# Optimization experiments

Measured on AMD Instinct MI355X. Metric: run time of the kernel, lower is better.

The kernel has to match this reference:

```python
import jax, jax.numpy as jnp
import numpy as np

B, DIM, H, W = 128, 640, 10, 10
M = H * W


def setup_inputs() -> dict:
    key = jax.random.key(0)
    x = jax.random.normal(key, (B, DIM, M), dtype=jnp.float32)
    # learned temperature parameter, init = log(1 / (2*h*w)), shape (1, 1)
    t = jnp.log(1.0 / (2 * H * W) * jnp.ones((1, 1), dtype=jnp.float32))
    return {"x": x, "t": t}


def reference(x, t):
    # x: [B, dim, M], t: [1, 1] temperature (log-scale)
    dim = x.shape[1]
    # Gram matrix x x^T: [B, dim, dim]
    xxT = jnp.einsum('bdm,bem->bde', x, x)
    # I_M.bmm(x_pow2*I) and (x_pow2*I).bmm(I_M) are just diagonal broadcasts
    d = jnp.diagonal(xxT, axis1=1, axis2=2)  # [B, dim]
    dcov = d[:, None, :] + d[:, :, None] - 2.0 * xxT
    dcov = jnp.maximum(dcov, 1e-4)
    dcov = jnp.sqrt(jnp.exp(t) * dcov + 1e-5)
    # double centering: dcov.bmm(I_M)/dim == row means, I_M.bmm(dcov)/dim == col means
    row_mean = jnp.mean(dcov, axis=2, keepdims=True)   # [B, dim, 1]
    col_mean = jnp.mean(dcov, axis=1, keepdims=True)   # [B, 1, dim]
    tot_mean = jnp.mean(dcov, axis=(1, 2), keepdims=True)  # [B, 1, 1]
    out = dcov - row_mean - col_mean + tot_mean
    return out.reshape(out.shape[0], dim * dim)
```

## Files before the change

kernel.cpp:

```cpp
#include <hip/hip_runtime.h>
#include <cmath>

#define NB    128
#define DIM_  640
#define MM    100
#define XHR   128
#define LDK   136
#define TFS   68
#define TTS   66
#define RSS   34
#define CSS   10

#define NWG   (NB * 55)
#define CPX   (NWG / 8)

typedef _Float16 half8 __attribute__((ext_vector_type(8)));
typedef float f32x4 __attribute__((ext_vector_type(4)));

__device__ inline void decode_bp(int bid, int& b, int& p) {
    const int dec = (bid & 7) * CPX + (bid >> 3);
    b = dec / 55;
    p = dec - b * 55;
}

__global__ __launch_bounds__(256) void prep_xh(const float* __restrict__ x,
                                               _Float16* __restrict__ xh,
                                               float* __restrict__ d,
                                               float* __restrict__ rmz) {
    if (blockIdx.x < 321) {
        const int z = blockIdx.x * 256 + threadIdx.x;
        if (z < 82048) rmz[z] = 0.f;
    }
    const int row  = blockIdx.x * 4 + (threadIdx.x >> 6);
    const int lane = threadIdx.x & 63;
    const float* xr = x + (size_t)row * MM;
    float2 v = make_float2(0.f, 0.f);
    if (lane < 50) v = *(const float2*)(xr + 2 * lane);
    const _Float16 h0 = (_Float16)v.x, h1 = (_Float16)v.y;
    const float a0 = (float)h0, a1 = (float)h1;
    float acc = a0 * a0 + a1 * a1;
    union { _Float16 h[2]; unsigned u; } pk;
    pk.h[0] = h0; pk.h[1] = h1;
    *(unsigned*)(xh + (size_t)row * XHR + 2 * lane) = pk.u;
    #pragma unroll
    for (int off = 32; off; off >>= 1) acc += __shfl_down(acc, off, 64);
    if (lane == 0) d[row] = acc;
}

__device__ inline void stage_xh(const _Float16* __restrict__ src,
                                _Float16* __restrict__ lds, int tid) {
    #pragma unroll
    for (int i = 0; i < 4; ++i) {
        const int idx = tid + i * 256;
        const int row = idx >> 4;
        const int m   = idx & 15;
        *(half8*)(lds + row * LDK + m * 8) = *(const half8*)(src + (size_t)row * XHR + m * 8);
    }
}

__global__ __launch_bounds__(256) void bdc_sums(
        const _Float16* __restrict__ xh, const float* __restrict__ d,
        const float* __restrict__ t, float* __restrict__ rm,
        float* __restrict__ tot) {
    __shared__ alignas(16) _Float16 As[64 * LDK];
    __shared__ alignas(16) _Float16 Bs[64 * LDK];
    float* rsum = (float*)As;
    float* csum = (float*)As + 64 * RSS;

    int b, p;
    decode_bp(blockIdx.x, b, p);
    int it = 0, rem = p;
    while (rem >= 10 - it) { rem -= 10 - it; ++it; }
    const int jt = it + rem;
    const bool diag = (it == jt);

    const int tid = threadIdx.x;
    const int wave = tid >> 6;
    const int lane = tid & 63;
    const int l16  = lane & 15;
    const int quad = lane >> 4;
    const int rowhalf = wave >> 1;
    const int colhalf = wave & 1;

    const _Float16* xb = xh + (size_t)b * DIM_ * XHR;
    stage_xh(xb + (size_t)(it * 64) * XHR, As, tid);
    if (!diag) stage_xh(xb + (size_t)(jt * 64) * XHR, Bs, tid);

    const float expt = expf(t[0]);
    const float* db = d + b * DIM_;
    const int rbase = it * 64 + rowhalf * 32;
    const int cbase = jt * 64 + colhalf * 32;
    float dr[2][4];
    #pragma unroll
    for (int ti = 0; ti < 2; ++ti)
        #pragma unroll
        for (int r = 0; r < 4; ++r)
            dr[ti][r] = db[rbase + ti * 16 + quad * 4 + r];
    const float dcv[2] = { db[cbase + l16], db[cbase + 16 + l16] };

    __syncthreads();

    const _Float16* Bp = diag ? As : Bs;
    f32x4 acc[2][2] = {};
    #pragma unroll
    for (int kk = 0; kk < 4; ++kk) {
        const int k = kk * 32 + quad * 8;
        half8 a0 = *(const half8*)(&As[(rowhalf * 32 + l16) * LDK + k]);
        half8 a1 = *(const half8*)(&As[(rowhalf * 32 + 16 + l16) * LDK + k]);
        half8 b0 = *(const half8*)(&Bp[(colhalf * 32 + l16) * LDK + k]);
        half8 b1 = *(const half8*)(&Bp[(colhalf * 32 + 16 + l16) * LDK + k]);
        acc[0][0] = __builtin_amdgcn_mfma_f32_16x16x32_f16(a0, b0, acc[0][0], 0, 0, 0);
        acc[0][1] = __builtin_amdgcn_mfma_f32_16x16x32_f16(a0, b1, acc[0][1], 0, 0, 0);
        acc[1][0] = __builtin_amdgcn_mfma_f32_16x16x32_f16(a1, b0, acc[1][0], 0, 0, 0);
        acc[1][1] = __builtin_amdgcn_mfma_f32_16x16x32_f16(a1, b1, acc[1][1], 0, 0, 0);
    }

    float s2[2][4];
    float cp0 = 0.f, cp1 = 0.f;
    #pragma unroll
    for (int ti = 0; ti < 2; ++ti) {
        #pragma unroll
        for (int r = 0; r < 4; ++r) {
            const int gi = rbase + ti * 16 + quad * 4 + r;
            float raw0 = dr[ti][r] + dcv[0] - 2.0f * acc[ti][0][r];
            raw0 = (gi == cbase + l16) ? 1e-4f : fmaxf(raw0, 1e-4f);
            const float v0 = sqrtf(expt * raw0 + 1e-5f);
            float raw1 = dr[ti][r] + dcv[1] - 2.0f * acc[ti][1][r];
            raw1 = (gi == cbase + 16 + l16) ? 1e-4f : fmaxf(raw1, 1e-4f);
            const float v1 = sqrtf(expt * raw1 + 1e-5f);
            s2[ti][r] = v0 + v1;
            cp0 += v0; cp1 += v1;
        }
    }

    __syncthreads();

    #pragma unroll
    for (int ti = 0; ti < 2; ++ti)
        #pragma unroll
        for (int r = 0; r < 4; ++r)
            rsum[(rowhalf * 32 + ti * 16 + quad * 4 + r) * RSS + colhalf * 16 + l16] = s2[ti][r];
    csum[(colhalf * 32 + l16) * CSS + rowhalf * 4 + quad]      = cp0;
    csum[(colhalf * 32 + 16 + l16) * CSS + rowhalf * 4 + quad] = cp1;

    __syncthreads();

    if (tid < 64) {
        float rt = 0.f;
        const float2* rp = (const float2*)(rsum + tid * RSS);
        #pragma unroll
        for (int k = 0; k < 16; ++k) { const float2 u = rp[k]; rt += u.x + u.y; }
        atomicAdd(&rm[b * DIM_ + it * 64 + tid], rt);
        float ts = rt;
        #pragma unroll
        for (int off = 1; off < 64; off <<= 1) ts += __shfl_xor(ts, off, 64);
        if (tid == 0) atomicAdd(&tot[b], diag ? ts : 2.0f * ts);
    } else if (tid < 128 && !diag) {
        const int c = tid - 64;
        float ct = 0.f;
        #pragma unroll
        for (int s = 0; s < 8; ++s) ct += csum[c * CSS + s];
        atomicAdd(&rm[b * DIM_ + jt * 64 + c], ct);
    }
}

__global__ __launch_bounds__(256) void bdc_out(
        const _Float16* __restrict__ xh, const float* __restrict__ d,
        const float* __restrict__ t, const float* __restrict__ rm,
        const float* __restrict__ tot_g, float* __restrict__ out) {
    __shared__ alignas(16) char uni[35200];
    _Float16* As = (_Float16*)uni;
    _Float16* Bs = (_Float16*)(uni + 17408);
    float* Tf = (float*)uni;
    float* Tt = (float*)(uni + 17408);
    __shared__ float rm_s[DIM_];

    int b, p;
    decode_bp(blockIdx.x, b, p);
    int it = 0, rem = p;
    while (rem >= 10 - it) { rem -= 10 - it; ++it; }
    const int jt = it + rem;
    const bool diag = (it == jt);

    const int tid  = threadIdx.x;
    const int wave = tid >> 6;
    const int lane = tid & 63;
    const int l16  = lane & 15;
    const int quad = lane >> 4;
    const int rowhalf = wave >> 1;
    const int colhalf = wave & 1;

    const _Float16* xb = xh + (size_t)b * DIM_ * XHR;
    stage_xh(xb + (size_t)(it * 64) * XHR, As, tid);
    if (!diag) stage_xh(xb + (size_t)(jt * 64) * XHR, Bs, tid);

    const float* rmg = rm + (size_t)b * DIM_;
    for (int i = tid; i < DIM_; i += 256) rm_s[i] = rmg[i] * (1.0f / 640.0f);
    const float tot = tot_g[b] * (1.0f / 409600.0f);

    const float expt = expf(t[0]);
    const float* db = d + b * DIM_;
    const int rbase = it * 64 + rowhalf * 32;
    const int cbase = jt * 64 + colhalf * 32;
    float dr[2][4];
    #pragma unroll
    for (int ti = 0; ti < 2; ++ti)
        #pragma unroll
        for (int r = 0; r < 4; ++r)
            dr[ti][r] = db[rbase + ti * 16 + quad * 4 + r];
    const float dcv[2] = { db[cbase + l16], db[cbase + 16 + l16] };

    __syncthreads();

    const _Float16* Bp = diag ? As : Bs;
    f32x4 acc[2][2] = {};
    #pragma unroll
    for (int kk = 0; kk < 4; ++kk) {
        const int k = kk * 32 + quad * 8;
        half8 a0 = *(const half8*)(&As[(rowhalf * 32 + l16) * LDK + k]);
        half8 a1 = *(const half8*)(&As[(rowhalf * 32 + 16 + l16) * LDK + k]);
        half8 b0 = *(const half8*)(&Bp[(colhalf * 32 + l16) * LDK + k]);
        half8 b1 = *(const half8*)(&Bp[(colhalf * 32 + 16 + l16) * LDK + k]);
        acc[0][0] = __builtin_amdgcn_mfma_f32_16x16x32_f16(a0, b0, acc[0][0], 0, 0, 0);
        acc[0][1] = __builtin_amdgcn_mfma_f32_16x16x32_f16(a0, b1, acc[0][1], 0, 0, 0);
        acc[1][0] = __builtin_amdgcn_mfma_f32_16x16x32_f16(a1, b0, acc[1][0], 0, 0, 0);
        acc[1][1] = __builtin_amdgcn_mfma_f32_16x16x32_f16(a1, b1, acc[1][1], 0, 0, 0);
    }

    float o[2][4][2];
    #pragma unroll
    for (int ti = 0; ti < 2; ++ti)
        #pragma unroll
        for (int r = 0; r < 4; ++r) {
            const int gi = rbase + ti * 16 + quad * 4 + r;
            const float rowterm = tot - rm_s[gi];
            #pragma unroll
            for (int tj = 0; tj < 2; ++tj) {
                const int gj = cbase + tj * 16 + l16;
                float raw = dr[ti][r] + dcv[tj] - 2.0f * acc[ti][tj][r];
                raw = (gi == gj) ? 1e-4f : fmaxf(raw, 1e-4f);
                o[ti][r][tj] = sqrtf(expt * raw + 1e-5f) + rowterm - rm_s[gj];
            }
        }

    __syncthreads();

    #pragma unroll
    for (int ti = 0; ti < 2; ++ti)
        #pragma unroll
        for (int r = 0; r < 4; ++r) {
            const int rowl = rowhalf * 32 + ti * 16 + quad * 4 + r;
            #pragma unroll
            for (int tj = 0; tj < 2; ++tj) {
                const int coll = colhalf * 32 + tj * 16 + l16;
                Tf[rowl * TFS + coll] = o[ti][r][tj];
                if (!diag)
                    Tt[coll * TTS + (rowl ^ ((l16 & 3) << 2))] = o[ti][r][tj];
            }
        }

    __syncthreads();

    float* ob = out + (size_t)b * DIM_ * DIM_;
    #pragma unroll
    for (int k4 = 0; k4 < 4; ++k4) {
        const int w  = tid + k4 * 256;
        const int rr = w >> 4;
        const int c4 = (w & 15) * 4;
        const f32x4 v = *(const f32x4*)(&Tf[rr * TFS + c4]);
        __builtin_nontemporal_store(v, (f32x4*)(ob + (size_t)(it * 64 + rr) * DIM_ + jt * 64 + c4));
    }
    if (!diag) {
        #pragma unroll
        for (int k4 = 0; k4 < 4; ++k4) {
            const int w  = tid + k4 * 256;
            const int rr = w >> 4;
            const int c4 = (w & 15) * 4;
            const int cc = c4 ^ ((rr & 3) << 2);
            const float2 p0 = *(const float2*)(&Tt[rr * TTS + cc]);
            const float2 p1 = *(const float2*)(&Tt[rr * TTS + cc + 2]);
            const f32x4 v = { p0.x, p0.y, p1.x, p1.y };
            __builtin_nontemporal_store(v, (f32x4*)(ob + (size_t)(jt * 64 + rr) * DIM_ + it * 64 + c4));
        }
    }
}

extern "C" void kernel_launch(void* const* d_in, const int* in_sizes, int n_in,
                              void* d_out, int out_size, void* d_ws, size_t ws_size,
                              hipStream_t stream) {
    const float* x = (const float*)d_in[0];
    const float* t = (const float*)d_in[1];
    float* out = (float*)d_out;

    char* ws = (char*)d_ws;
    _Float16* xh = (_Float16*)ws;
    float*    d  = (float*)(ws + 20971520);
    float*    rm = (float*)(ws + 20971520 + 327680);
    float*    tot= (float*)(ws + 20971520 + 2 * 327680);

    prep_xh<<<dim3(NB * DIM_ / 4), dim3(256), 0, stream>>>(x, xh, d, rm);
    bdc_sums<<<dim3(NWG), dim3(256), 0, stream>>>(xh, d, t, rm, tot);
    bdc_out<<<dim3(NWG), dim3(256), 0, stream>>>(xh, d, t, rm, tot, out);
}
```

Baseline: 275.5 us.

## Switch to row-panel blocks looping over all column tiles with double-buffered staging

Each workgroup now owns a 64-row panel and walks all ten column tiles, double-buffering the B tile in LDS and keeping A fragments in registers. Row sums are written directly, which removes the atomics, the zeroing pass and the symmetric column-sum path. The output kernel computes the full 64x640 panel without the transpose trick and stores results straight from registers, dropping the LDS staging of outputs. The price is that symmetry is no longer exploited, so both the Gram matrix and the sqrt work double. The grid also drops to 1280 workgroups, and the direct stores are scalar 4-byte writes where the old code issued 16-byte stores.

```diff
diff --git a/kernel.cpp b/kernel.cpp
--- a/kernel.cpp
+++ b/kernel.cpp
@@ -6,31 +6,27 @@
 #define MM    100
 #define XHR   128
 #define LDK   136
-#define TFS   68
-#define TTS   66
 #define RSS   34
-#define CSS   10
-
-#define NWG   (NB * 55)
-#define CPX   (NWG / 8)
+
+#define NWG2  (NB * 10)
+#define CPX2  (NWG2 / 8)
 
 typedef _Float16 half8 __attribute__((ext_vector_type(8)));
 typedef float f32x4 __attribute__((ext_vector_type(4)));
 
-__device__ inline void decode_bp(int bid, int& b, int& p) {
-    const int dec = (bid & 7) * CPX + (bid >> 3);
-    b = dec / 55;
-    p = dec - b * 55;
+#define FSQRT(x) __builtin_amdgcn_sqrtf(x)
+
+#define MFMA16(a, bb, c) __builtin_amdgcn_mfma_f32_16x16x32_f16(a, bb, c, 0, 0, 0)
+
+__device__ inline void decode_bp10(int bid, int& b, int& pnl) {
+    const int dec = (bid & 7) * CPX2 + (bid >> 3);
+    b = dec / 10;
+    pnl = dec - b * 10;
 }
 
 __global__ __launch_bounds__(256) void prep_xh(const float* __restrict__ x,
                                                _Float16* __restrict__ xh,
-                                               float* __restrict__ d,
-                                               float* __restrict__ rmz) {
-    if (blockIdx.x < 321) {
-        const int z = blockIdx.x * 256 + threadIdx.x;
-        if (z < 82048) rmz[z] = 0.f;
-    }
+                                               float* __restrict__ d) {
     const int row  = blockIdx.x * 4 + (threadIdx.x >> 6);
     const int lane = threadIdx.x & 63;
     const float* xr = x + (size_t)row * MM;
@@ -61,18 +57,13 @@
 __global__ __launch_bounds__(256) void bdc_sums(
         const _Float16* __restrict__ xh, const float* __restrict__ d,
         const float* __restrict__ t, float* __restrict__ rm,
-        float* __restrict__ tot) {
+        float* __restrict__ totpart) {
     __shared__ alignas(16) _Float16 As[64 * LDK];
-    __shared__ alignas(16) _Float16 Bs[64 * LDK];
+    __shared__ alignas(16) _Float16 Bs[2][64 * LDK];
     float* rsum = (float*)As;
-    float* csum = (float*)As + 64 * RSS;
-
-    int b, p;
-    decode_bp(blockIdx.x, b, p);
-    int it = 0, rem = p;
-    while (rem >= 10 - it) { rem -= 10 - it; ++it; }
-    const int jt = it + rem;
-    const bool diag = (it == jt);
+
+    int b, it;
+    decode_bp10(blockIdx.x, b, it);
 
     const int tid = threadIdx.x;
     const int wave = tid >> 6;
@@ -84,64 +75,69 @@
 
     const _Float16* xb = xh + (size_t)b * DIM_ * XHR;
     stage_xh(xb + (size_t)(it * 64) * XHR, As, tid);
-    if (!diag) stage_xh(xb + (size_t)(jt * 64) * XHR, Bs, tid);
-
-    const float expt = expf(t[0]);
+    stage_xh(xb, Bs[0], tid);
+
+    const float expt = __expf(t[0]);
     const float* db = d + b * DIM_;
     const int rbase = it * 64 + rowhalf * 32;
-    const int cbase = jt * 64 + colhalf * 32;
     float dr[2][4];
     #pragma unroll
     for (int ti = 0; ti < 2; ++ti)
         #pragma unroll
         for (int r = 0; r < 4; ++r)
             dr[ti][r] = db[rbase + ti * 16 + quad * 4 + r];
-    const float dcv[2] = { db[cbase + l16], db[cbase + 16 + l16] };
 
     __syncthreads();
 
-    const _Float16* Bp = diag ? As : Bs;
-    f32x4 acc[2][2] = {};
+    half8 af[2][4];
     #pragma unroll
     for (int kk = 0; kk < 4; ++kk) {
         const int k = kk * 32 + quad * 8;
-        half8 a0 = *(const half8*)(&As[(rowhalf * 32 + l16) * LDK + k]);
-        half8 a1 = *(const half8*)(&As[(rowhalf * 32 + 16 + l16) * LDK + k]);
-        half8 b0 = *(const half8*)(&Bp[(colhalf * 32 + l16) * LDK + k]);
-        half8 b1 = *(const half8*)(&Bp[(colhalf * 32 + 16 + l16) * LDK + k]);
-        acc[0][0] = __builtin_amdgcn_mfma_f32_16x16x32_f16(a0, b0, acc[0][0], 0, 0, 0);
-        acc[0][1] = __builtin_amdgcn_mfma_f32_16x16x32_f16(a0, b1, acc[0][1], 0, 0, 0);
-        acc[1][0] = __builtin_amdgcn_mfma_f32_16x16x32_f16(a1, b0, acc[1][0], 0, 0, 0);
-        acc[1][1] = __builtin_amdgcn_mfma_f32_16x16x32_f16(a1, b1, acc[1][1], 0, 0, 0);
-    }
-
-    float s2[2][4];
-    float cp0 = 0.f, cp1 = 0.f;
-    #pragma unroll
-    for (int ti = 0; ti < 2; ++ti) {
-        #pragma unroll
-        for (int r = 0; r < 4; ++r) {
-            const int gi = rbase + ti * 16 + quad * 4 + r;
-            float raw0 = dr[ti][r] + dcv[0] - 2.0f * acc[ti][0][r];
-            raw0 = (gi == cbase + l16) ? 1e-4f : fmaxf(raw0, 1e-4f);
-            const float v0 = sqrtf(expt * raw0 + 1e-5f);
-            float raw1 = dr[ti][r] + dcv[1] - 2.0f * acc[ti][1][r];
-            raw1 = (gi == cbase + 16 + l16) ? 1e-4f : fmaxf(raw1, 1e-4f);
-            const float v1 = sqrtf(expt * raw1 + 1e-5f);
-            s2[ti][r] = v0 + v1;
-            cp0 += v0; cp1 += v1;
+        af[0][kk] = *(const half8*)(&As[(rowhalf * 32 + l16) * LDK + k]);
+        af[1][kk] = *(const half8*)(&As[(rowhalf * 32 + 16 + l16) * LDK + k]);
+    }
+
+    float rowpart[2][4] = {};
+    for (int jt = 0; jt < 10; ++jt) {
+        const int cur = jt & 1;
+        if (jt < 9) stage_xh(xb + (size_t)((jt + 1) * 64) * XHR, Bs[cur ^ 1], tid);
+
+        const int cbase = jt * 64 + colhalf * 32;
+        const float dcv0 = db[cbase + l16];
+        const float dcv1 = db[cbase + 16 + l16];
+
+        const _Float16* Bp = Bs[cur];
+        f32x4 acc[2][2] = {};
+        #pragma unroll
+        for (int kk = 0; kk < 4; ++kk) {
+            const int k = kk * 32 + quad * 8;
+            half8 b0 = *(const half8*)(&Bp[(colhalf * 32 + l16) * LDK + k]);
+            half8 b1 = *(const half8*)(&Bp[(colhalf * 32 + 16 + l16) * LDK + k]);
+            acc[0][0] = MFMA16(af[0][kk], b0, acc[0][0]);
+            acc[0][1] = MFMA16(af[0][kk], b1, acc[0][1]);
+            acc[1][0] = MFMA16(af[1][kk], b0, acc[1][0]);
+            acc[1][1] = MFMA16(af[1][kk], b1, acc[1][1]);
         }
-    }
-
-    __syncthreads();
+
+        #pragma unroll
+        for (int ti = 0; ti < 2; ++ti)
+            #pragma unroll
+            for (int r = 0; r < 4; ++r) {
+                const int gi = rbase + ti * 16 + quad * 4 + r;
+                float raw0 = dr[ti][r] + dcv0 - 2.0f * acc[ti][0][r];
+                raw0 = (gi == cbase + l16) ? 1e-4f : fmaxf(raw0, 1e-4f);
+                float raw1 = dr[ti][r] + dcv1 - 2.0f * acc[ti][1][r];
+                raw1 = (gi == cbase + 16 + l16) ? 1e-4f : fmaxf(raw1, 1e-4f);
+                rowpart[ti][r] += FSQRT(expt * raw0 + 1e-5f) + FSQRT(expt * raw1 + 1e-5f);
+            }
+        __syncthreads();
+    }
 
     #pragma unroll
     for (int ti = 0; ti < 2; ++ti)
         #pragma unroll
         for (int r = 0; r < 4; ++r)
-            rsum[(rowhalf * 32 + ti * 16 + quad * 4 + r) * RSS + colhalf * 16 + l16] = s2[ti][r];
-    csum[(colhalf * 32 + l16) * CSS + rowhalf * 4 + quad]      = cp0;
-    csum[(colhalf * 32 + 16 + l16) * CSS + rowhalf * 4 + quad] = cp1;
+            rsum[(rowhalf * 32 + ti * 16 + quad * 4 + r) * RSS + colhalf * 16 + l16] = rowpart[ti][r];
 
     __syncthreads();
 
@@ -150,39 +146,25 @@
         const float2* rp = (const float2*)(rsum + tid * RSS);
         #pragma unroll
         for (int k = 0; k < 16; ++k) { const float2 u = rp[k]; rt += u.x + u.y; }
-        atomicAdd(&rm[b * DIM_ + it * 64 + tid], rt);
+        rm[b * DIM_ + it * 64 + tid] = rt;
         float ts = rt;
         #pragma unroll
         for (int off = 1; off < 64; off <<= 1) ts += __shfl_xor(ts, off, 64);
-        if (tid == 0) atomicAdd(&tot[b], diag ? ts : 2.0f * ts);
-    } else if (tid < 128 && !diag) {
-        const int c = tid - 64;
-        float ct = 0.f;
-        #pragma unroll
-        for (int s = 0; s < 8; ++s) ct += csum[c * CSS + s];
-        atomicAdd(&rm[b * DIM_ + jt * 64 + c], ct);
+        if (tid == 0) totpart[b * 10 + it] = ts;
     }
 }
 
 __global__ __launch_bounds__(256) void bdc_out(
         const _Float16* __restrict__ xh, const float* __restrict__ d,
         const float* __restrict__ t, const float* __restrict__ rm,
-        const float* __restrict__ tot_g, float* __restrict__ out) {
-    __shared__ alignas(16) char uni[35200];
-    _Float16* As = (_Float16*)uni;
-    _Float16* Bs = (_Float16*)(uni + 17408);
-    float* Tf = (float*)uni;
-    float* Tt = (float*)(uni + 17408);
-    __shared__ float rm_s[DIM_];
-
-    int b, p;
-    decode_bp(blockIdx.x, b, p);
-    int it = 0, rem = p;
-    while (rem >= 10 - it) { rem -= 10 - it; ++it; }
-    const int jt = it + rem;
-    const bool diag = (it == jt);
-
-    const int tid  = threadIdx.x;
+        const float* __restrict__ totpart, float* __restrict__ out) {
+    __shared__ alignas(16) _Float16 As[64 * LDK];
+    __shared__ alignas(16) _Float16 Bs[2][64 * LDK];
+
+    int b, it;
+    decode_bp10(blockIdx.x, b, it);
+
+    const int tid = threadIdx.x;
     const int wave = tid >> 6;
     const int lane = tid & 63;
     const int l16  = lane & 15;
@@ -192,96 +174,80 @@
 
     const _Float16* xb = xh + (size_t)b * DIM_ * XHR;
     stage_xh(xb + (size_t)(it * 64) * XHR, As, tid);
-    if (!diag) stage_xh(xb + (size_t)(jt * 64) * XHR, Bs, tid);
-
+    stage_xh(xb, Bs[0], tid);
+
+    const float expt = __expf(t[0]);
+    const float* db  = d + b * DIM_;
     const float* rmg = rm + (size_t)b * DIM_;
-    for (int i = tid; i < DIM_; i += 256) rm_s[i] = rmg[i] * (1.0f / 640.0f);
-    const float tot = tot_g[b] * (1.0f / 409600.0f);
-
-    const float expt = expf(t[0]);
-    const float* db = d + b * DIM_;
+
+    float tp = 0.f;
+    #pragma unroll
+    for (int s = 0; s < 10; ++s) tp += totpart[b * 10 + s];
+    const float tot = tp * (1.0f / 409600.0f);
+
     const int rbase = it * 64 + rowhalf * 32;
-    const int cbase = jt * 64 + colhalf * 32;
-    float dr[2][4];
+    float dr[2][4], rmi[2][4];
     #pragma unroll
     for (int ti = 0; ti < 2; ++ti)
         #pragma unroll
-        for (int r = 0; r < 4; ++r)
-            dr[ti][r] = db[rbase + ti * 16 + quad * 4 + r];
-    const float dcv[2] = { db[cbase + l16], db[cbase + 16 + l16] };
+        for (int r = 0; r < 4; ++r) {
+            const int gi = rbase + ti * 16 + quad * 4 + r;
+            dr[ti][r]  = db[gi];
+            rmi[ti][r] = tot - rmg[gi] * (1.0f / 640.0f);
+        }
 
     __syncthreads();
 
-    const _Float16* Bp = diag ? As : Bs;
-    f32x4 acc[2][2] = {};
+    half8 af[2][4];
     #pragma unroll
     for (int kk = 0; kk < 4; ++kk) {
         const int k = kk * 32 + quad * 8;
-        half8 a0 = *(const half8*)(&As[(rowhalf * 32 + l16) * LDK + k]);
-        half8 a1 = *(const half8*)(&As[(rowhalf * 32 + 16 + l16) * LDK + k]);
-        half8 b0 = *(const half8*)(&Bp[(colhalf * 32 + l16) * LDK + k]);
-        half8 b1 = *(const half8*)(&Bp[(colhalf * 32 + 16 + l16) * LDK + k]);
-        acc[0][0] = __builtin_amdgcn_mfma_f32_16x16x32_f16(a0, b0, acc[0][0], 0, 0, 0);
-        acc[0][1] = __builtin_amdgcn_mfma_f32_16x16x32_f16(a0, b1, acc[0][1], 0, 0, 0);
-        acc[1][0] = __builtin_amdgcn_mfma_f32_16x16x32_f16(a1, b0, acc[1][0], 0, 0, 0);
-        acc[1][1] = __builtin_amdgcn_mfma_f32_16x16x32_f16(a1, b1, acc[1][1], 0, 0, 0);
-    }
-
-    float o[2][4][2];
-    #pragma unroll
-    for (int ti = 0; ti < 2; ++ti)
-        #pragma unroll
-        for (int r = 0; r < 4; ++r) {
-            const int gi = rbase + ti * 16 + quad * 4 + r;
-            const float rowterm = tot - rm_s[gi];
+        af[0][kk] = *(const half8*)(&As[(rowhalf * 32 + l16) * LDK + k]);
+        af[1][kk] = *(const half8*)(&As[(rowhalf * 32 + 16 + l16) * LDK + k]);
+    }
+
+    float* obr = out + ((size_t)b * DIM_ + it * 64 + rowhalf * 32) * DIM_;
+
+    for (int jt = 0; jt < 10; ++jt) {
+        const int cur = jt & 1;
+        if (jt < 9) stage_xh(xb + (size_t)((jt + 1) * 64) * XHR, Bs[cur ^ 1], tid);
+
+        const int cbase = jt * 64 + colhalf * 32;
+        const float dcv0 = db[cbase + l16];
+        const float dcv1 = db[cbase + 16 + l16];
+        const float rmj0 = rmg[cbase + l16]      * (1.0f / 640.0f);
+        const float rmj1 = rmg[cbase + 16 + l16] * (1.0f / 640.0f);
+
+        const _Float16* Bp = Bs[cur];
+        f32x4 acc[2][2] = {};
+        #pragma unroll
+        for (int kk = 0; kk < 4; ++kk) {
+            const int k = kk * 32 + quad * 8;
+            half8 b0 = *(const half8*)(&Bp[(colhalf * 32 + l16) * LDK + k]);
+            half8 b1 = *(const half8*)(&Bp[(colhalf * 32 + 16 + l16) * LDK + k]);
+            acc[0][0] = MFMA16(af[0][kk], b0, acc[0][0]);
+            acc[0][1] = MFMA16(af[0][kk], b1, acc[0][1]);
+            acc[1][0] = MFMA16(af[1][kk], b0, acc[1][0]);
+            acc[1][1] = MFMA16(af[1][kk], b1, acc[1][1]);
+        }
+
+        #pragma unroll
+        for (int ti = 0; ti < 2; ++ti)
             #pragma unroll
-            for (int tj = 0; tj < 2; ++tj) {
-                const int gj = cbase + tj * 16 + l16;
-                float raw = dr[ti][r] + dcv[tj] - 2.0f * acc[ti][tj][r];
-                raw = (gi == gj) ? 1e-4f : fmaxf(raw, 1e-4f);
-                o[ti][r][tj] = sqrtf(expt * raw + 1e-5f) + rowterm - rm_s[gj];
+            for (int r = 0; r < 4; ++r) {
+                const int rowl = ti * 16 + quad * 4 + r;
+                const int gi = rbase + rowl;
+                float raw0 = dr[ti][r] + dcv0 - 2.0f * acc[ti][0][r];
+                raw0 = (gi == cbase + l16) ? 1e-4f : fmaxf(raw0, 1e-4f);
+                const float o0 = FSQRT(expt * raw0 + 1e-5f) + rmi[ti][r] - rmj0;
+                float raw1 = dr[ti][r] + dcv1 - 2.0f * acc[ti][1][r];
+                raw1 = (gi == cbase + 16 + l16) ? 1e-4f : fmaxf(raw1, 1e-4f);
+                const float o1 = FSQRT(expt * raw1 + 1e-5f) + rmi[ti][r] - rmj1;
+                float* rp = obr + (size_t)rowl * DIM_ + cbase;
+                __builtin_nontemporal_store(o0, rp + l16);
+                __builtin_nontemporal_store(o1, rp + 16 + l16);
             }
-        }
-
-    __syncthreads();
-
-    #pragma unroll
-    for (int ti = 0; ti < 2; ++ti)
-        #pragma unroll
-        for (int r = 0; r < 4; ++r) {
-            const int rowl = rowhalf * 32 + ti * 16 + quad * 4 + r;
-            #pragma unroll
-            for (int tj = 0; tj < 2; ++tj) {
-                const int coll = colhalf * 32 + tj * 16 + l16;
-                Tf[rowl * TFS + coll] = o[ti][r][tj];
-                if (!diag)
-                    Tt[coll * TTS + (rowl ^ ((l16 & 3) << 2))] = o[ti][r][tj];
-            }
-        }
-
-    __syncthreads();
-
-    float* ob = out + (size_t)b * DIM_ * DIM_;
-    #pragma unroll
-    for (int k4 = 0; k4 < 4; ++k4) {
-        const int w  = tid + k4 * 256;
-        const int rr = w >> 4;
-        const int c4 = (w & 15) * 4;
-        const f32x4 v = *(const f32x4*)(&Tf[rr * TFS + c4]);
-        __builtin_nontemporal_store(v, (f32x4*)(ob + (size_t)(it * 64 + rr) * DIM_ + jt * 64 + c4));
-    }
-    if (!diag) {
-        #pragma unroll
-        for (int k4 = 0; k4 < 4; ++k4) {
-            const int w  = tid + k4 * 256;
-            const int rr = w >> 4;
-            const int c4 = (w & 15) * 4;
-            const int cc = c4 ^ ((rr & 3) << 2);
-            const float2 p0 = *(const float2*)(&Tt[rr * TTS + cc]);
-            const float2 p1 = *(const float2*)(&Tt[rr * TTS + cc + 2]);
-            const f32x4 v = { p0.x, p0.y, p1.x, p1.y };
-            __builtin_nontemporal_store(v, (f32x4*)(ob + (size_t)(jt * 64 + rr) * DIM_ + it * 64 + c4));
-        }
+        __syncthreads();
     }
 }
 
@@ -293,12 +259,12 @@
     float* out = (float*)d_out;
 
     char* ws = (char*)d_ws;
-    _Float16* xh = (_Float16*)ws;
-    float*    d  = (float*)(ws + 20971520);
-    float*    rm = (float*)(ws + 20971520 + 327680);
-    float*    tot= (float*)(ws + 20971520 + 2 * 327680);
-
-    prep_xh<<<dim3(NB * DIM_ / 4), dim3(256), 0, stream>>>(x, xh, d, rm);
-    bdc_sums<<<dim3(NWG), dim3(256), 0, stream>>>(xh, d, t, rm, tot);
-    bdc_out<<<dim3(NWG), dim3(256), 0, stream>>>(xh, d, t, rm, tot, out);
-}
+    _Float16* xh  = (_Float16*)ws;
+    float*    d   = (float*)(ws + 20971520);
+    float*    rm  = (float*)(ws + 20971520 + 327680);
+    float*    tpp = (float*)(ws + 20971520 + 2 * 327680);
+
+    prep_xh<<<dim3(NB * DIM_ / 4), dim3(256), 0, stream>>>(x, xh, d);
+    bdc_sums<<<dim3(NWG2), dim3(256), 0, stream>>>(xh, d, t, rm, tpp);
+    bdc_out<<<dim3(NWG2), dim3(256), 0, stream>>>(xh, d, t, rm, tpp, out);
+}
```

Result: slower. 286.6 us (+4.0%).
